# Performance work log

Hardware: AMD Instinct MI355X
Metric: run time of the kernel (lower is better)

## Reference

```python
import jax, jax.numpy as jnp
import numpy as np

DT = 0.01
STEPS = 30
D = 2048


def setup_inputs() -> dict:
    key = jax.random.key(0)
    ks = jax.random.split(key, 7)
    B, S = 4, 4096
    x = jax.random.normal(ks[0], (B, S, D), jnp.float32)
    lorenz = jnp.array([10.0, 28.0, 8.0 / 3.0], jnp.float32)
    strength = jnp.float32(0.3)
    W_in = jax.random.normal(ks[1], (3, D), jnp.float32) / np.sqrt(D)
    b_in = jax.random.normal(ks[2], (3,), jnp.float32) * 0.01
    W_out = jax.random.normal(ks[3], (D, 18), jnp.float32) / np.sqrt(18.0)
    b_out = jax.random.normal(ks[4], (D,), jnp.float32) * 0.01
    return {"x": x, "lorenz": lorenz, "strength": strength,
            "W_in": W_in, "b_in": b_in, "W_out": W_out, "b_out": b_out}


def _deriv(s, sigma, rho, beta):
    xx, yy, zz = s[..., 0], s[..., 1], s[..., 2]
    return jnp.stack([sigma * (yy - xx), xx * (rho - zz) - yy, xx * yy - beta * zz], axis=-1)


def reference(x, lorenz, strength, W_in, b_in, W_out, b_out):
    orig_shape = x.shape
    xf = x.reshape(-1, x.shape[-1])            # [N, D]
    state0 = xf @ W_in.T + b_in                # [N, 3]
    params = jnp.clip(jnp.abs(lorenz), 0.1, None)
    sigma, rho, beta = params[0], params[1], params[2]

    def step(s, _):
        k1 = _deriv(s, sigma, rho, beta)
        k2 = _deriv(s + 0.5 * DT * k1, sigma, rho, beta)
        k3 = _deriv(s + 0.5 * DT * k2, sigma, rho, beta)
        k4 = _deriv(s + DT * k3, sigma, rho, beta)
        s2 = s + (DT / 6.0) * (k1 + 2.0 * k2 + 2.0 * k3 + k4)
        return s2, s2

    _, ys = jax.lax.scan(step, state0, None, length=STEPS)  # [STEPS, N, 3]
    traj = jnp.concatenate([state0[:, None], jnp.moveaxis(ys, 0, 1)], axis=1)  # [N, STEPS+1, 3]

    feats = jnp.concatenate([
        traj[:, 0],                         # initial state
        traj[:, -1],                        # final state
        traj.mean(axis=1),
        traj.std(axis=1, ddof=1),           # torch.std is unbiased by default
        traj.min(axis=1),
        traj.max(axis=1),
    ], axis=-1)                             # [N, 18]

    pert = feats @ W_out.T + b_out          # [N, D]
    out = xf + jnp.tanh(pert) * jnp.abs(strength)
    return out.reshape(orig_shape)
```

## Files before the change

kernel.cpp:

```cpp
#include <hip/hip_runtime.h>
#include <math.h>

#define DD 2048
#define DTC 0.01f
#define NSTEPS 30
#define ROWS 4

__device__ __forceinline__ void lorenz_deriv(float x, float y, float z,
                                             float sigma, float rho, float beta,
                                             float& dx, float& dy, float& dz) {
    dx = sigma * (y - x);
    dy = x * (rho - z) - y;
    dz = x * y - beta * z;
}

__device__ __forceinline__ float fast_tanh(float p) {
    float e = __expf(2.0f * p);
    return 1.0f - __fdividef(2.0f, e + 1.0f);
}

__global__ __launch_bounds__(256) void fused_enrich(
    const float* __restrict__ x, const float* __restrict__ lorenz,
    const float* __restrict__ W_in, const float* __restrict__ b_in,
    const float* __restrict__ W_out, const float* __restrict__ b_out,
    const float* __restrict__ strength, float* __restrict__ out) {
    __shared__ float x_tile[ROWS * DD];
    __shared__ float red[4][ROWS * 3];
    __shared__ float st0[ROWS][3];
    __shared__ float feats_lds[ROWS][20];

    const int tid = threadIdx.x;
    const int lane = tid & 63;
    const int wv = tid >> 6;
    const int row0 = blockIdx.x * ROWS;
    const int d0 = tid * 8;

    float w0[8], w1[8], w2[8];
    {
        const float4* p0 = reinterpret_cast<const float4*>(W_in + 0 * DD + d0);
        const float4* p1 = reinterpret_cast<const float4*>(W_in + 1 * DD + d0);
        const float4* p2 = reinterpret_cast<const float4*>(W_in + 2 * DD + d0);
        float4 a, b;
        a = p0[0]; b = p0[1];
        w0[0]=a.x; w0[1]=a.y; w0[2]=a.z; w0[3]=a.w; w0[4]=b.x; w0[5]=b.y; w0[6]=b.z; w0[7]=b.w;
        a = p1[0]; b = p1[1];
        w1[0]=a.x; w1[1]=a.y; w1[2]=a.z; w1[3]=a.w; w1[4]=b.x; w1[5]=b.y; w1[6]=b.z; w1[7]=b.w;
        a = p2[0]; b = p2[1];
        w2[0]=a.x; w2[1]=a.y; w2[2]=a.z; w2[3]=a.w; w2[4]=b.x; w2[5]=b.y; w2[6]=b.z; w2[7]=b.w;
    }

    {
        const float* gbase = x + (size_t)row0 * DD;
#pragma unroll
        for (int i = 0; i < 8; ++i) {
            const int foff = wv * 2048 + i * 256;
            __builtin_amdgcn_global_load_lds(
                (const __attribute__((address_space(1))) unsigned int*)(gbase + foff + lane * 4),
                (__attribute__((address_space(3))) unsigned int*)(x_tile + foff),
                16, 0, 0);
        }
    }
    __syncthreads();

    float part[ROWS][3];
#pragma unroll
    for (int r = 0; r < ROWS; ++r) {
        const float4* p = reinterpret_cast<const float4*>(x_tile + r * DD + d0);
        float4 a = p[0], b = p[1];
        float xv[8] = {a.x, a.y, a.z, a.w, b.x, b.y, b.z, b.w};
        float s0 = 0.f, s1 = 0.f, s2 = 0.f;
#pragma unroll
        for (int j = 0; j < 8; ++j) {
            s0 += xv[j] * w0[j];
            s1 += xv[j] * w1[j];
            s2 += xv[j] * w2[j];
        }
        part[r][0] = s0; part[r][1] = s1; part[r][2] = s2;
    }

#pragma unroll
    for (int r = 0; r < ROWS; ++r) {
#pragma unroll
        for (int k = 0; k < 3; ++k) {
            float v = part[r][k];
#pragma unroll
            for (int off = 32; off > 0; off >>= 1) v += __shfl_xor(v, off, 64);
            if (lane == 0) red[wv][r * 3 + k] = v;
        }
    }
    __syncthreads();
    if (tid < ROWS * 3) {
        float v = red[0][tid] + red[1][tid] + red[2][tid] + red[3][tid] + b_in[tid % 3];
        st0[tid / 3][tid % 3] = v;
    }
    __syncthreads();

    if (tid < ROWS) {
        const float sigma = fmaxf(fabsf(lorenz[0]), 0.1f);
        const float rho   = fmaxf(fabsf(lorenz[1]), 0.1f);
        const float beta  = fmaxf(fabsf(lorenz[2]), 0.1f);
        float sx = st0[tid][0], sy = st0[tid][1], sz = st0[tid][2];
        const float ix = sx, iy = sy, iz = sz;
        float sux = sx, suy = sy, suz = sz;
        float sqx = sx * sx, sqy = sy * sy, sqz = sz * sz;
        float mnx = sx, mny = sy, mnz = sz;
        float mxx = sx, mxy = sy, mxz = sz;
#pragma unroll 1
        for (int t = 0; t < NSTEPS; ++t) {
            float k1x, k1y, k1z, k2x, k2y, k2z, k3x, k3y, k3z, k4x, k4y, k4z;
            float ax, ay, az;
            lorenz_deriv(sx, sy, sz, sigma, rho, beta, k1x, k1y, k1z);
            ax = sx + 0.5f * DTC * k1x; ay = sy + 0.5f * DTC * k1y; az = sz + 0.5f * DTC * k1z;
            lorenz_deriv(ax, ay, az, sigma, rho, beta, k2x, k2y, k2z);
            ax = sx + 0.5f * DTC * k2x; ay = sy + 0.5f * DTC * k2y; az = sz + 0.5f * DTC * k2z;
            lorenz_deriv(ax, ay, az, sigma, rho, beta, k3x, k3y, k3z);
            ax = sx + DTC * k3x; ay = sy + DTC * k3y; az = sz + DTC * k3z;
            lorenz_deriv(ax, ay, az, sigma, rho, beta, k4x, k4y, k4z);
            sx += (DTC / 6.0f) * (k1x + 2.0f * k2x + 2.0f * k3x + k4x);
            sy += (DTC / 6.0f) * (k1y + 2.0f * k2y + 2.0f * k3y + k4y);
            sz += (DTC / 6.0f) * (k1z + 2.0f * k2z + 2.0f * k3z + k4z);
            sux += sx; suy += sy; suz += sz;
            sqx += sx * sx; sqy += sy * sy; sqz += sz * sz;
            mnx = fminf(mnx, sx); mny = fminf(mny, sy); mnz = fminf(mnz, sz);
            mxx = fmaxf(mxx, sx); mxy = fmaxf(mxy, sy); mxz = fmaxf(mxz, sz);
        }
        const float inv31 = 1.0f / 31.0f;
        const float inv30 = 1.0f / 30.0f;
        const float mex = sux * inv31, mey = suy * inv31, mez = suz * inv31;
        const float vax = fmaxf((sqx - sux * mex) * inv30, 0.0f);
        const float vay = fmaxf((sqy - suy * mey) * inv30, 0.0f);
        const float vaz = fmaxf((sqz - suz * mez) * inv30, 0.0f);
        float* f = feats_lds[tid];
        f[0]  = ix;  f[1]  = iy;  f[2]  = iz;
        f[3]  = sx;  f[4]  = sy;  f[5]  = sz;
        f[6]  = mex; f[7]  = mey; f[8]  = mez;
        f[9]  = sqrtf(vax); f[10] = sqrtf(vay); f[11] = sqrtf(vaz);
        f[12] = mnx; f[13] = mny; f[14] = mnz;
        f[15] = mxx; f[16] = mxy; f[17] = mxz;
    }
    __syncthreads();

    float f[ROWS][18];
#pragma unroll
    for (int r = 0; r < ROWS; ++r)
#pragma unroll
        for (int k = 0; k < 18; ++k) f[r][k] = feats_lds[r][k];

    const float sabs = fabsf(strength[0]);
#pragma unroll 1
    for (int j = 0; j < 8; ++j) {
        const int c = tid + j * 256;
        float w[18];
        {
            const float2* wp2 = reinterpret_cast<const float2*>(W_out + (size_t)c * 18);
#pragma unroll
            for (int k = 0; k < 9; ++k) { float2 t = wp2[k]; w[2*k] = t.x; w[2*k+1] = t.y; }
        }
        const float bo = b_out[c];
#pragma unroll
        for (int r = 0; r < ROWS; ++r) {
            float p = bo;
#pragma unroll
            for (int k = 0; k < 18; ++k) p += f[r][k] * w[k];
            const float xv = x_tile[r * DD + c];
            out[(size_t)(row0 + r) * DD + c] = xv + fast_tanh(p) * sabs;
        }
    }
}

extern "C" void kernel_launch(void* const* d_in, const int* in_sizes, int n_in,
                              void* d_out, int out_size, void* d_ws, size_t ws_size,
                              hipStream_t stream) {
    const float* x        = (const float*)d_in[0];
    const float* lorenz   = (const float*)d_in[1];
    const float* strength = (const float*)d_in[2];
    const float* W_in     = (const float*)d_in[3];
    const float* b_in     = (const float*)d_in[4];
    const float* W_out    = (const float*)d_in[5];
    const float* b_out    = (const float*)d_in[6];
    float* out = (float*)d_out;

    const int N = in_sizes[0] / DD;

    fused_enrich<<<N / ROWS, 256, 0, stream>>>(
        x, lorenz, W_in, b_in, W_out, b_out, strength, out);
}
```

Measured before the change: 88.09 us.

## Keep x tile in registers, transpose W_out, vectorize output with nontemporal stores

A small pre-kernel transposes W_out into the workspace so each thread can read contiguous float4 weight columns. The main kernel now holds the x tile in registers instead of staging it in LDS, so occupancy can rise (launch bounds 256,4), and it computes the 8 contiguous output columns per thread with vector FMAs. The RK4 integration moves to a single wavefront chosen per block, and the output is written with nontemporal float4 stores. The cost is an extra kernel launch and workspace traffic for the transpose, which is redone on every call.

```diff
diff --git a/kernel.cpp b/kernel.cpp
--- a/kernel.cpp
+++ b/kernel.cpp
@@ -5,6 +5,8 @@
 #define DTC 0.01f
 #define NSTEPS 30
 #define ROWS 4
+
+typedef float floatx4 __attribute__((ext_vector_type(4)));
 
 __device__ __forceinline__ void lorenz_deriv(float x, float y, float z,
                                              float sigma, float rho, float beta,
@@ -19,152 +21,156 @@
     return 1.0f - __fdividef(2.0f, e + 1.0f);
 }
 
-__global__ __launch_bounds__(256) void fused_enrich(
+__global__ __launch_bounds__(256) void k_transpose(const float* __restrict__ W_out,
+                                                   float* __restrict__ wsT) {
+    const int oidx = blockIdx.x * 256 + threadIdx.x;
+    const int k = oidx >> 11;
+    const int c = oidx & 2047;
+    wsT[oidx] = W_out[c * 18 + k];
+}
+
+__global__ __launch_bounds__(256, 4) void fused2(
     const float* __restrict__ x, const float* __restrict__ lorenz,
     const float* __restrict__ W_in, const float* __restrict__ b_in,
-    const float* __restrict__ W_out, const float* __restrict__ b_out,
+    const float* __restrict__ wsT, const float* __restrict__ b_out,
     const float* __restrict__ strength, float* __restrict__ out) {
-    __shared__ float x_tile[ROWS * DD];
     __shared__ float red[4][ROWS * 3];
-    __shared__ float st0[ROWS][3];
-    __shared__ float feats_lds[ROWS][20];
+    __shared__ float feats_lds[ROWS][18];
 
     const int tid = threadIdx.x;
     const int lane = tid & 63;
     const int wv = tid >> 6;
     const int row0 = blockIdx.x * ROWS;
-    const int d0 = tid * 8;
+    const int c0 = tid * 8;
 
-    float w0[8], w1[8], w2[8];
-    {
-        const float4* p0 = reinterpret_cast<const float4*>(W_in + 0 * DD + d0);
-        const float4* p1 = reinterpret_cast<const float4*>(W_in + 1 * DD + d0);
-        const float4* p2 = reinterpret_cast<const float4*>(W_in + 2 * DD + d0);
-        float4 a, b;
-        a = p0[0]; b = p0[1];
-        w0[0]=a.x; w0[1]=a.y; w0[2]=a.z; w0[3]=a.w; w0[4]=b.x; w0[5]=b.y; w0[6]=b.z; w0[7]=b.w;
-        a = p1[0]; b = p1[1];
-        w1[0]=a.x; w1[1]=a.y; w1[2]=a.z; w1[3]=a.w; w1[4]=b.x; w1[5]=b.y; w1[6]=b.z; w1[7]=b.w;
-        a = p2[0]; b = p2[1];
-        w2[0]=a.x; w2[1]=a.y; w2[2]=a.z; w2[3]=a.w; w2[4]=b.x; w2[5]=b.y; w2[6]=b.z; w2[7]=b.w;
+    floatx4 xva[ROWS], xvb[ROWS];
+#pragma unroll
+    for (int r = 0; r < ROWS; ++r) {
+        const float* p = x + (size_t)(row0 + r) * DD + c0;
+        xva[r] = *reinterpret_cast<const floatx4*>(p);
+        xvb[r] = *reinterpret_cast<const floatx4*>(p + 4);
     }
 
+    floatx4 wa0, wb0, wa1, wb1, wa2, wb2;
     {
-        const float* gbase = x + (size_t)row0 * DD;
+        const float* p0 = W_in + 0 * DD + c0;
+        const float* p1 = W_in + 1 * DD + c0;
+        const float* p2 = W_in + 2 * DD + c0;
+        wa0 = *reinterpret_cast<const floatx4*>(p0); wb0 = *reinterpret_cast<const floatx4*>(p0 + 4);
+        wa1 = *reinterpret_cast<const floatx4*>(p1); wb1 = *reinterpret_cast<const floatx4*>(p1 + 4);
+        wa2 = *reinterpret_cast<const floatx4*>(p2); wb2 = *reinterpret_cast<const floatx4*>(p2 + 4);
+    }
+
 #pragma unroll
-        for (int i = 0; i < 8; ++i) {
-            const int foff = wv * 2048 + i * 256;
-            __builtin_amdgcn_global_load_lds(
-                (const __attribute__((address_space(1))) unsigned int*)(gbase + foff + lane * 4),
-                (__attribute__((address_space(3))) unsigned int*)(x_tile + foff),
-                16, 0, 0);
+    for (int r = 0; r < ROWS; ++r) {
+        floatx4 s0 = xva[r] * wa0 + xvb[r] * wb0;
+        floatx4 s1 = xva[r] * wa1 + xvb[r] * wb1;
+        floatx4 s2 = xva[r] * wa2 + xvb[r] * wb2;
+        float v0 = s0.x + s0.y + s0.z + s0.w;
+        float v1 = s1.x + s1.y + s1.z + s1.w;
+        float v2 = s2.x + s2.y + s2.z + s2.w;
+#pragma unroll
+        for (int off = 32; off > 0; off >>= 1) {
+            v0 += __shfl_xor(v0, off, 64);
+            v1 += __shfl_xor(v1, off, 64);
+            v2 += __shfl_xor(v2, off, 64);
+        }
+        if (lane == 0) {
+            red[wv][r * 3 + 0] = v0;
+            red[wv][r * 3 + 1] = v1;
+            red[wv][r * 3 + 2] = v2;
         }
     }
     __syncthreads();
 
-    float part[ROWS][3];
-#pragma unroll
-    for (int r = 0; r < ROWS; ++r) {
-        const float4* p = reinterpret_cast<const float4*>(x_tile + r * DD + d0);
-        float4 a = p[0], b = p[1];
-        float xv[8] = {a.x, a.y, a.z, a.w, b.x, b.y, b.z, b.w};
-        float s0 = 0.f, s1 = 0.f, s2 = 0.f;
-#pragma unroll
-        for (int j = 0; j < 8; ++j) {
-            s0 += xv[j] * w0[j];
-            s1 += xv[j] * w1[j];
-            s2 += xv[j] * w2[j];
+    if (wv == (int)(blockIdx.x & 3)) {
+        float v = 0.0f;
+        if (lane < ROWS * 3) {
+            v = red[0][lane] + red[1][lane] + red[2][lane] + red[3][lane]
+                + b_in[lane % 3];
         }
-        part[r][0] = s0; part[r][1] = s1; part[r][2] = s2;
-    }
-
-#pragma unroll
-    for (int r = 0; r < ROWS; ++r) {
-#pragma unroll
-        for (int k = 0; k < 3; ++k) {
-            float v = part[r][k];
-#pragma unroll
-            for (int off = 32; off > 0; off >>= 1) v += __shfl_xor(v, off, 64);
-            if (lane == 0) red[wv][r * 3 + k] = v;
+        float sx = __shfl(v, lane * 3 + 0, 64);
+        float sy = __shfl(v, lane * 3 + 1, 64);
+        float sz = __shfl(v, lane * 3 + 2, 64);
+        if (lane < ROWS) {
+            const float sigma = fmaxf(fabsf(lorenz[0]), 0.1f);
+            const float rho   = fmaxf(fabsf(lorenz[1]), 0.1f);
+            const float beta  = fmaxf(fabsf(lorenz[2]), 0.1f);
+            const float ix = sx, iy = sy, iz = sz;
+            float sux = sx, suy = sy, suz = sz;
+            float sqx = sx * sx, sqy = sy * sy, sqz = sz * sz;
+            float mnx = sx, mny = sy, mnz = sz;
+            float mxx = sx, mxy = sy, mxz = sz;
+#pragma unroll 1
+            for (int t = 0; t < NSTEPS; ++t) {
+                float k1x, k1y, k1z, k2x, k2y, k2z, k3x, k3y, k3z, k4x, k4y, k4z;
+                float ax, ay, az;
+                lorenz_deriv(sx, sy, sz, sigma, rho, beta, k1x, k1y, k1z);
+                ax = sx + 0.5f * DTC * k1x; ay = sy + 0.5f * DTC * k1y; az = sz + 0.5f * DTC * k1z;
+                lorenz_deriv(ax, ay, az, sigma, rho, beta, k2x, k2y, k2z);
+                ax = sx + 0.5f * DTC * k2x; ay = sy + 0.5f * DTC * k2y; az = sz + 0.5f * DTC * k2z;
+                lorenz_deriv(ax, ay, az, sigma, rho, beta, k3x, k3y, k3z);
+                ax = sx + DTC * k3x; ay = sy + DTC * k3y; az = sz + DTC * k3z;
+                lorenz_deriv(ax, ay, az, sigma, rho, beta, k4x, k4y, k4z);
+                sx += (DTC / 6.0f) * (k1x + 2.0f * k2x + 2.0f * k3x + k4x);
+                sy += (DTC / 6.0f) * (k1y + 2.0f * k2y + 2.0f * k3y + k4y);
+                sz += (DTC / 6.0f) * (k1z + 2.0f * k2z + 2.0f * k3z + k4z);
+                sux += sx; suy += sy; suz += sz;
+                sqx += sx * sx; sqy += sy * sy; sqz += sz * sz;
+                mnx = fminf(mnx, sx); mny = fminf(mny, sy); mnz = fminf(mnz, sz);
+                mxx = fmaxf(mxx, sx); mxy = fmaxf(mxy, sy); mxz = fmaxf(mxz, sz);
+            }
+            const float inv31 = 1.0f / 31.0f;
+            const float inv30 = 1.0f / 30.0f;
+            const float mex = sux * inv31, mey = suy * inv31, mez = suz * inv31;
+            const float vax = fmaxf((sqx - sux * mex) * inv30, 0.0f);
+            const float vay = fmaxf((sqy - suy * mey) * inv30, 0.0f);
+            const float vaz = fmaxf((sqz - suz * mez) * inv30, 0.0f);
+            float* f = feats_lds[lane];
+            f[0]  = ix;  f[1]  = iy;  f[2]  = iz;
+            f[3]  = sx;  f[4]  = sy;  f[5]  = sz;
+            f[6]  = mex; f[7]  = mey; f[8]  = mez;
+            f[9]  = sqrtf(vax); f[10] = sqrtf(vay); f[11] = sqrtf(vaz);
+            f[12] = mnx; f[13] = mny; f[14] = mnz;
+            f[15] = mxx; f[16] = mxy; f[17] = mxz;
         }
     }
     __syncthreads();
-    if (tid < ROWS * 3) {
-        float v = red[0][tid] + red[1][tid] + red[2][tid] + red[3][tid] + b_in[tid % 3];
-        st0[tid / 3][tid % 3] = v;
-    }
-    __syncthreads();
-
-    if (tid < ROWS) {
-        const float sigma = fmaxf(fabsf(lorenz[0]), 0.1f);
-        const float rho   = fmaxf(fabsf(lorenz[1]), 0.1f);
-        const float beta  = fmaxf(fabsf(lorenz[2]), 0.1f);
-        float sx = st0[tid][0], sy = st0[tid][1], sz = st0[tid][2];
-        const float ix = sx, iy = sy, iz = sz;
-        float sux = sx, suy = sy, suz = sz;
-        float sqx = sx * sx, sqy = sy * sy, sqz = sz * sz;
-        float mnx = sx, mny = sy, mnz = sz;
-        float mxx = sx, mxy = sy, mxz = sz;
-#pragma unroll 1
-        for (int t = 0; t < NSTEPS; ++t) {
-            float k1x, k1y, k1z, k2x, k2y, k2z, k3x, k3y, k3z, k4x, k4y, k4z;
-            float ax, ay, az;
-            lorenz_deriv(sx, sy, sz, sigma, rho, beta, k1x, k1y, k1z);
-            ax = sx + 0.5f * DTC * k1x; ay = sy + 0.5f * DTC * k1y; az = sz + 0.5f * DTC * k1z;
-            lorenz_deriv(ax, ay, az, sigma, rho, beta, k2x, k2y, k2z);
-            ax = sx + 0.5f * DTC * k2x; ay = sy + 0.5f * DTC * k2y; az = sz + 0.5f * DTC * k2z;
-            lorenz_deriv(ax, ay, az, sigma, rho, beta, k3x, k3y, k3z);
-            ax = sx + DTC * k3x; ay = sy + DTC * k3y; az = sz + DTC * k3z;
-            lorenz_deriv(ax, ay, az, sigma, rho, beta, k4x, k4y, k4z);
-            sx += (DTC / 6.0f) * (k1x + 2.0f * k2x + 2.0f * k3x + k4x);
-            sy += (DTC / 6.0f) * (k1y + 2.0f * k2y + 2.0f * k3y + k4y);
-            sz += (DTC / 6.0f) * (k1z + 2.0f * k2z + 2.0f * k3z + k4z);
-            sux += sx; suy += sy; suz += sz;
-            sqx += sx * sx; sqy += sy * sy; sqz += sz * sz;
-            mnx = fminf(mnx, sx); mny = fminf(mny, sy); mnz = fminf(mnz, sz);
-            mxx = fmaxf(mxx, sx); mxy = fmaxf(mxy, sy); mxz = fmaxf(mxz, sz);
-        }
-        const float inv31 = 1.0f / 31.0f;
-        const float inv30 = 1.0f / 30.0f;
-        const float mex = sux * inv31, mey = suy * inv31, mez = suz * inv31;
-        const float vax = fmaxf((sqx - sux * mex) * inv30, 0.0f);
-        const float vay = fmaxf((sqy - suy * mey) * inv30, 0.0f);
-        const float vaz = fmaxf((sqz - suz * mez) * inv30, 0.0f);
-        float* f = feats_lds[tid];
-        f[0]  = ix;  f[1]  = iy;  f[2]  = iz;
-        f[3]  = sx;  f[4]  = sy;  f[5]  = sz;
-        f[6]  = mex; f[7]  = mey; f[8]  = mez;
-        f[9]  = sqrtf(vax); f[10] = sqrtf(vay); f[11] = sqrtf(vaz);
-        f[12] = mnx; f[13] = mny; f[14] = mnz;
-        f[15] = mxx; f[16] = mxy; f[17] = mxz;
-    }
-    __syncthreads();
-
-    float f[ROWS][18];
-#pragma unroll
-    for (int r = 0; r < ROWS; ++r)
-#pragma unroll
-        for (int k = 0; k < 18; ++k) f[r][k] = feats_lds[r][k];
 
     const float sabs = fabsf(strength[0]);
-#pragma unroll 1
-    for (int j = 0; j < 8; ++j) {
-        const int c = tid + j * 256;
-        float w[18];
-        {
-            const float2* wp2 = reinterpret_cast<const float2*>(W_out + (size_t)c * 18);
+    floatx4 pa[ROWS], pb[ROWS];
+    {
+        const floatx4 boa = *reinterpret_cast<const floatx4*>(b_out + c0);
+        const floatx4 bob = *reinterpret_cast<const floatx4*>(b_out + c0 + 4);
 #pragma unroll
-            for (int k = 0; k < 9; ++k) { float2 t = wp2[k]; w[2*k] = t.x; w[2*k+1] = t.y; }
-        }
-        const float bo = b_out[c];
+        for (int r = 0; r < ROWS; ++r) { pa[r] = boa; pb[r] = bob; }
+    }
+#pragma unroll
+    for (int k = 0; k < 18; ++k) {
+        const float* wp = wsT + k * DD + c0;
+        const floatx4 wka = *reinterpret_cast<const floatx4*>(wp);
+        const floatx4 wkb = *reinterpret_cast<const floatx4*>(wp + 4);
 #pragma unroll
         for (int r = 0; r < ROWS; ++r) {
-            float p = bo;
+            const float fk = feats_lds[r][k];
+            pa[r] += fk * wka;
+            pb[r] += fk * wkb;
+        }
+    }
 #pragma unroll
-            for (int k = 0; k < 18; ++k) p += f[r][k] * w[k];
-            const float xv = x_tile[r * DD + c];
-            out[(size_t)(row0 + r) * DD + c] = xv + fast_tanh(p) * sabs;
-        }
+    for (int r = 0; r < ROWS; ++r) {
+        floatx4 oa, ob;
+        oa.x = xva[r].x + fast_tanh(pa[r].x) * sabs;
+        oa.y = xva[r].y + fast_tanh(pa[r].y) * sabs;
+        oa.z = xva[r].z + fast_tanh(pa[r].z) * sabs;
+        oa.w = xva[r].w + fast_tanh(pa[r].w) * sabs;
+        ob.x = xvb[r].x + fast_tanh(pb[r].x) * sabs;
+        ob.y = xvb[r].y + fast_tanh(pb[r].y) * sabs;
+        ob.z = xvb[r].z + fast_tanh(pb[r].z) * sabs;
+        ob.w = xvb[r].w + fast_tanh(pb[r].w) * sabs;
+        float* op = out + (size_t)(row0 + r) * DD + c0;
+        __builtin_nontemporal_store(oa, reinterpret_cast<floatx4*>(op));
+        __builtin_nontemporal_store(ob, reinterpret_cast<floatx4*>(op + 4));
     }
 }
 
@@ -179,9 +185,11 @@
     const float* W_out    = (const float*)d_in[5];
     const float* b_out    = (const float*)d_in[6];
     float* out = (float*)d_out;
+    float* wsT = (float*)d_ws;
 
     const int N = in_sizes[0] / DD;
 
-    fused_enrich<<<N / ROWS, 256, 0, stream>>>(
-        x, lorenz, W_in, b_in, W_out, b_out, strength, out);
+    k_transpose<<<(18 * DD) / 256, 256, 0, stream>>>(W_out, wsT);
+    fused2<<<N / ROWS, 256, 0, stream>>>(
+        x, lorenz, W_in, b_in, wsT, b_out, strength, out);
 }
```

Measured after the change: 91.66 us. +4.1%, slower.
